# Performance work log

Measured on AMD Instinct MI355X. Metric: run time of the kernel, lower is better.

Reference implementation:

```python
import jax, jax.numpy as jnp
import numpy as np

N_HEAD = 16
N_KV_HEADS = 4
HEAD_DIM = 64  # n_emb // n_head = 1024 // 16
WINDOW = 512
NEG_INF = float('-inf')


def _rope_tables(T, dim, dtype):
    inv_freq = 1.0 / (10000.0 ** (jnp.arange(0, dim, 2, dtype=jnp.float32) / dim))
    t = jnp.arange(T, dtype=jnp.float32)
    freqs = jnp.einsum('i,j->ij', t, inv_freq)          # [T, dim/2]
    emb = jnp.concatenate((freqs, freqs), axis=-1)       # [T, dim]
    return jnp.cos(emb).astype(dtype), jnp.sin(emb).astype(dtype)


def _apply_rope(x, cos, sin):
    # x: [B, H, T, D]; cos/sin: [T, D]
    x1, x2 = jnp.split(x, 2, axis=-1)
    x_rot = jnp.concatenate((-x2, x1), axis=-1)
    return x * cos + x_rot * sin


def setup_inputs() -> dict:
    key = jax.random.key(0)
    ks = jax.random.split(key, 5)
    B, T, C = 1, 4096, 1024
    kv_dim = N_KV_HEADS * HEAD_DIM
    s = 0.02
    return {
        'x': jax.random.normal(ks[0], (B, T, C), jnp.float32),
        'wq': jax.random.normal(ks[1], (C, C), jnp.float32) * s,
        'wk': jax.random.normal(ks[2], (kv_dim, C), jnp.float32) * s,
        'wv': jax.random.normal(ks[3], (kv_dim, C), jnp.float32) * s,
        'wo': jax.random.normal(ks[4], (C, C), jnp.float32) * s,
    }


def reference(x, wq, wk, wv, wo):
    B, T, C = x.shape
    n_rep = N_HEAD // N_KV_HEADS
    # QKV projections (torch Linear: x @ W.T)
    q = (x @ wq.T).reshape(B, T, N_HEAD, HEAD_DIM).transpose(0, 2, 1, 3)      # [B,H,T,D]
    k = (x @ wk.T).reshape(B, T, N_KV_HEADS, HEAD_DIM).transpose(0, 2, 1, 3)  # [B,Hkv,T,D]
    v = (x @ wv.T).reshape(B, T, N_KV_HEADS, HEAD_DIM).transpose(0, 2, 1, 3)
    # RoPE
    cos, sin = _rope_tables(T, HEAD_DIM, x.dtype)
    q = _apply_rope(q, cos, sin)
    k = _apply_rope(k, cos, sin)
    # GQA: repeat KV heads
    k = jnp.repeat(k, n_rep, axis=1)  # [B,H,T,D]
    v = jnp.repeat(v, n_rep, axis=1)
    # Sliding-window causal mask: allow j <= i and j > i - WINDOW
    i = jnp.arange(T)[:, None]
    j = jnp.arange(T)[None, :]
    allowed = (j <= i) & (j > i - WINDOW)  # [T,T]
    scale = 1.0 / np.sqrt(HEAD_DIM)
    scores = jnp.einsum('bhqd,bhkd->bhqk', q, k) * scale
    scores = jnp.where(allowed[None, None], scores, NEG_INF)
    attn = jax.nn.softmax(scores, axis=-1)
    y = jnp.einsum('bhqk,bhkd->bhqd', attn, v)            # [B,H,T,D]
    y = y.transpose(0, 2, 1, 3).reshape(B, T, C)
    return y @ wo.T
```

## Files before the change

### kernel.cpp

```cpp
#include <hip/hip_runtime.h>
#include <hip/hip_bf16.h>
#include <stdint.h>

#define T_SEQ 4096
#define CDIM  1024
#define NH    16
#define NKV   4
#define HD    64
#define WIN   512
#define KVD   256
#define QKVN  1536

typedef unsigned short ushort_t;
typedef __attribute__((ext_vector_type(8))) __bf16 bf16x8;
typedef __attribute__((ext_vector_type(4))) float  f32x4;
typedef __attribute__((ext_vector_type(4))) unsigned short us4;
typedef __attribute__((ext_vector_type(8))) unsigned short us8;

__device__ inline unsigned short f2bf(float f) {
  unsigned u = __builtin_bit_cast(unsigned, f);
  u += 0x7fffu + ((u >> 16) & 1u);
  return (unsigned short)(u >> 16);
}

__device__ inline unsigned cvt_pk_bf16(float lo, float hi) {
  unsigned r;
  asm("v_cvt_pk_bf16_f32 %0, %1, %2" : "=v"(r) : "v"(lo), "v"(hi));
  return r;
}

__device__ inline f32x4 mfma16(bf16x8 a, bf16x8 b, f32x4 c) {
  return __builtin_amdgcn_mfma_f32_16x16x32_bf16(a, b, c, 0, 0, 0);
}

__device__ inline void load_lds16(const void* g, void* s) {
  __builtin_amdgcn_global_load_lds(
      (const __attribute__((address_space(1))) void*)g,
      (__attribute__((address_space(3))) void*)s, 16, 0, 0);
}

__global__ __launch_bounds__(256) void prep_kernel(
    const float* __restrict__ x,  const float* __restrict__ wq,
    const float* __restrict__ wk, const float* __restrict__ wv,
    const float* __restrict__ wo,
    ushort_t* __restrict__ xb, ushort_t* __restrict__ wqkvb,
    ushort_t* __restrict__ wob,
    float* __restrict__ ct, float* __restrict__ st) {
  const int NX  = T_SEQ * CDIM / 8;
  const int NWQ = CDIM * CDIM / 8;
  const int NWK = KVD * CDIM / 8;
  const int NCONV = NX + 2 * NWQ + 2 * NWK;
  int i = blockIdx.x * 256 + threadIdx.x;
  if (i >= NCONV) {
    int j = i - NCONV;
    if (j >= T_SEQ * 32) return;
    int t = j >> 5, f = j & 31;
    float inv = __builtin_exp2f(-(float)f * (13.287712379549449f / 32.0f));
    float a = (float)t * inv;
    ct[j] = cosf(a);
    st[j] = sinf(a);
    return;
  }
  const float4* src; ushort_t* dst; int off;
  if (i < NX)                        { src = (const float4*)x;  dst = xb;                              off = i; }
  else if (i < NX + NWQ)             { src = (const float4*)wq; dst = wqkvb;                           off = i - NX; }
  else if (i < NX + NWQ + NWK)       { src = (const float4*)wk; dst = wqkvb + CDIM * CDIM;             off = i - NX - NWQ; }
  else if (i < NX + NWQ + 2 * NWK)   { src = (const float4*)wv; dst = wqkvb + CDIM * CDIM + KVD * CDIM; off = i - NX - NWQ - NWK; }
  else                               { src = (const float4*)wo; dst = wob;                             off = i - NX - NWQ - 2 * NWK; }
  float4 v0 = src[off * 2], v1 = src[off * 2 + 1];
  us8 o;
  o[0] = f2bf(v0.x); o[1] = f2bf(v0.y); o[2] = f2bf(v0.z); o[3] = f2bf(v0.w);
  o[4] = f2bf(v1.x); o[5] = f2bf(v1.y); o[6] = f2bf(v1.z); o[7] = f2bf(v1.w);
  *(us8*)(dst + (size_t)off * 8) = o;
}

template <int EPI>
__global__ __launch_bounds__(256) void gemm_kernel(
    const ushort_t* __restrict__ A, const ushort_t* __restrict__ B, int K,
    float* __restrict__ outF,
    ushort_t* __restrict__ qbuf, ushort_t* __restrict__ kbuf, ushort_t* __restrict__ vt,
    const float* __restrict__ ct, const float* __restrict__ st) {
  __shared__ __align__(16) ushort_t smA[2][64 * 64];
  __shared__ __align__(16) ushort_t smB[2][128 * 64];
  const int tid = threadIdx.x, lane = tid & 63, wid = tid >> 6;

  const int id = blockIdx.x + (gridDim.x * blockIdx.y);
  const int nwg = gridDim.x * gridDim.y;
  const int swz = (id & 7) * (nwg >> 3) + (id >> 3);
  const int bm = (swz & 63) * 64, bn = (swz >> 6) * 128;

  const int wr = wid >> 1, wc = wid & 1;
  const int l15 = lane & 15, lg = lane >> 4;
  const int r8 = lane >> 3;
  const int cc = lane & 7;
  const int scc = (cc ^ r8) * 8;

  f32x4 acc[2][4];
#pragma unroll
  for (int i = 0; i < 2; i++)
#pragma unroll
    for (int j = 0; j < 4; j++) acc[i][j] = (f32x4)0.0f;

#define GSTAGE(buf, ktv)                                                                              \
  do {                                                                                                \
    load_lds16(A + (size_t)(bm + wid * 8 + r8) * K + (ktv) + scc, (char*)smA[buf] + wid * 1024);                 \
    load_lds16(A + (size_t)(bm + (wid + 4) * 8 + r8) * K + (ktv) + scc, (char*)smA[buf] + (wid + 4) * 1024);     \
    load_lds16(B + (size_t)(bn + wid * 8 + r8) * K + (ktv) + scc, (char*)smB[buf] + wid * 1024);                 \
    load_lds16(B + (size_t)(bn + (wid + 4) * 8 + r8) * K + (ktv) + scc, (char*)smB[buf] + (wid + 4) * 1024);     \
    load_lds16(B + (size_t)(bn + (wid + 8) * 8 + r8) * K + (ktv) + scc, (char*)smB[buf] + (wid + 8) * 1024);     \
    load_lds16(B + (size_t)(bn + (wid + 12) * 8 + r8) * K + (ktv) + scc, (char*)smB[buf] + (wid + 12) * 1024);   \
  } while (0)

  GSTAGE(0, 0);
  const int NK = K / 64;
  int cur = 0;
  for (int kt = 0; kt < NK; ++kt) {
    if (kt + 1 < NK) {
      GSTAGE(cur ^ 1, (kt + 1) * 64);
      asm volatile("s_waitcnt vmcnt(6)" ::: "memory");
    } else {
      asm volatile("s_waitcnt vmcnt(0)" ::: "memory");
    }
    __builtin_amdgcn_sched_barrier(0);
    __builtin_amdgcn_s_barrier();
    __builtin_amdgcn_sched_barrier(0);

    bf16x8 af[2][2], bfr[4][2];
#pragma unroll
    for (int mi = 0; mi < 2; mi++) {
      int r = wr * 32 + mi * 16 + l15, sw8 = r & 7;
#pragma unroll
      for (int ks = 0; ks < 2; ks++)
        af[mi][ks] = *(const bf16x8*)&smA[cur][r * 64 + ((ks * 4 + lg) ^ sw8) * 8];
    }
#pragma unroll
    for (int ni = 0; ni < 4; ni++) {
      int r = wc * 64 + ni * 16 + l15, sw8 = r & 7;
#pragma unroll
      for (int ks = 0; ks < 2; ks++)
        bfr[ni][ks] = *(const bf16x8*)&smB[cur][r * 64 + ((ks * 4 + lg) ^ sw8) * 8];
    }
#pragma unroll
    for (int ks = 0; ks < 2; ks++)
#pragma unroll
      for (int mi = 0; mi < 2; mi++)
#pragma unroll
        for (int ni = 0; ni < 4; ni++)
          acc[mi][ni] = mfma16(af[mi][ks], bfr[ni][ks], acc[mi][ni]);

    __builtin_amdgcn_sched_barrier(0);
    __builtin_amdgcn_s_barrier();
    __builtin_amdgcn_sched_barrier(0);
    cur ^= 1;
  }
#undef GSTAGE

  const int col0 = bn + wc * 64;
  if (EPI == 1) {
#pragma unroll
    for (int mi = 0; mi < 2; mi++) {
      int r0 = bm + wr * 32 + mi * 16 + lg * 4;
#pragma unroll
      for (int ni = 0; ni < 4; ni++) {
        int c = col0 + ni * 16 + l15;
#pragma unroll
        for (int r = 0; r < 4; r++) outF[(size_t)(r0 + r) * CDIM + c] = acc[mi][ni][r];
      }
    }
  } else {
    if (col0 < CDIM + KVD) {
      bool isQ = (col0 < CDIM);
      ushort_t* obuf = isQ ? qbuf : kbuf;
      int ostride = isQ ? CDIM : KVD;
      int obase = isQ ? col0 : col0 - CDIM;
#pragma unroll
      for (int mi = 0; mi < 2; mi++) {
        int r0 = bm + wr * 32 + mi * 16 + lg * 4;
#pragma unroll
        for (int ni = 0; ni < 2; ni++) {
          int dd = ni * 16 + l15;
#pragma unroll
          for (int r = 0; r < 4; r++) {
            int t = r0 + r;
            float c_ = ct[t * 32 + dd], s_ = st[t * 32 + dd];
            float lo = acc[mi][ni][r], hi = acc[mi][ni + 2][r];
            obuf[(size_t)t * ostride + obase + dd]      = f2bf(lo * c_ - hi * s_);
            obuf[(size_t)t * ostride + obase + dd + 32] = f2bf(hi * c_ + lo * s_);
          }
        }
      }
    } else {
#pragma unroll
      for (int mi = 0; mi < 2; mi++) {
        int t0 = bm + wr * 32 + mi * 16 + lg * 4;
#pragma unroll
        for (int ni = 0; ni < 4; ni++) {
          int cv = col0 + ni * 16 + l15 - (CDIM + KVD);
          us4 o;
          o.x = f2bf(acc[mi][ni][0]); o.y = f2bf(acc[mi][ni][1]);
          o.z = f2bf(acc[mi][ni][2]); o.w = f2bf(acc[mi][ni][3]);
          *(us4*)&vt[(size_t)cv * T_SEQ + t0] = o;
        }
      }
    }
  }
}

__global__ __launch_bounds__(256, 4) void attn_kernel(
    const ushort_t* __restrict__ qbuf, const ushort_t* __restrict__ kbuf,
    const ushort_t* __restrict__ vt, ushort_t* __restrict__ ybuf) {
  __shared__ __align__(16) ushort_t smK[2][64 * 64];
  __shared__ __align__(16) ushort_t smV[2][64 * 64];
  const int tid = threadIdx.x, lane = tid & 63, wid = tid >> 6;
  const int l15 = lane & 15, lg = lane >> 4;
  const int blk = blockIdx.x;
  const int h  = (blk & 7) * 2 + ((blk >> 3) & 1);
  const int qb = (blk >> 4) * 64;
  const int kvh = h >> 2;
  const int qbw = qb + wid * 16;

  const int r8 = lane >> 3;
  const int cc = lane & 7;
  const int sc = ((cc ^ r8) * 8);
  const int ra = wid * 8 + r8;
  const int rb = (wid + 4) * 8 + r8;

  int kb0 = qb - (WIN - 1);
  if (kb0 < 0) kb0 = 0;
  kb0 &= ~63;
  const int nt = ((qb + 63) - kb0) / 64 + 1;

#define STAGE(buf, kbase)                                                                  \
  do {                                                                                     \
    load_lds16(kbuf + (size_t)((kbase) + ra) * KVD + kvh * HD + sc, (char*)smK[buf] + wid * 1024);        \
    load_lds16(kbuf + (size_t)((kbase) + rb) * KVD + kvh * HD + sc, (char*)smK[buf] + (wid + 4) * 1024);  \
    load_lds16(vt + (size_t)(kvh * HD + ra) * T_SEQ + (kbase) + sc, (char*)smV[buf] + wid * 1024);        \
    load_lds16(vt + (size_t)(kvh * HD + rb) * T_SEQ + (kbase) + sc, (char*)smV[buf] + (wid + 4) * 1024);  \
  } while (0)

  STAGE(0, kb0);

  const ushort_t* qrow = qbuf + (size_t)(qbw + l15) * CDIM + h * HD;
  bf16x8 qf0 = *(const bf16x8*)(qrow + lg * 8);
  bf16x8 qf1 = *(const bf16x8*)(qrow + 32 + lg * 8);

  f32x4 o[4];
#pragma unroll
  for (int j = 0; j < 4; j++) o[j] = (f32x4)0.f;
  float lpart = 0.f;
  const float SC = 0.125f * 1.4426950408889634f;
  const int sw = l15 & 7;

  int cur = 0;
  for (int t = 0; t < nt; ++t) {
    const int kb = kb0 + t * 64;
    if (t + 1 < nt) {
      STAGE(cur ^ 1, kb + 64);
      asm volatile("s_waitcnt vmcnt(4)" ::: "memory");
    } else {
      asm volatile("s_waitcnt vmcnt(0)" ::: "memory");
    }
    __builtin_amdgcn_sched_barrier(0);
    __builtin_amdgcn_s_barrier();
    __builtin_amdgcn_sched_barrier(0);

    if (kb <= qbw + 15) {
      const ushort_t* sk = smK[cur];
      const ushort_t* sv_ = smV[cur];

      f32x4 s[4];
      __builtin_amdgcn_s_setprio(1);
#pragma unroll
      for (int g = 0; g < 4; g++) {
        bf16x8 k0 = *(const bf16x8*)&sk[(g * 16 + l15) * 64 + ((lg ^ sw) * 8)];
        bf16x8 k1 = *(const bf16x8*)&sk[(g * 16 + l15) * 64 + (((4 + lg) ^ sw) * 8)];
        s[g] = mfma16(k0, qf0, (f32x4)0.f);
        s[g] = mfma16(k1, qf1, s[g]);
      }
      __builtin_amdgcn_s_setprio(0);

      const bool nomask = (kb + 63 <= qbw) && (kb > qbw + 15 - WIN);
      unsigned pw[8];
      {
        const int q = qbw + l15;
        float ps = 0.f;
#pragma unroll
        for (int g = 0; g < 4; g++) {
          float p0, p1, p2, p3;
          if (nomask) {
            p0 = __builtin_exp2f(s[g][0] * SC);
            p1 = __builtin_exp2f(s[g][1] * SC);
            p2 = __builtin_exp2f(s[g][2] * SC);
            p3 = __builtin_exp2f(s[g][3] * SC);
          } else {
            int k0 = kb + g * 16 + lg * 4;
            p0 = __builtin_exp2f((k0 + 0 <= q && k0 + 0 > q - WIN) ? s[g][0] * SC : -3e38f);
            p1 = __builtin_exp2f((k0 + 1 <= q && k0 + 1 > q - WIN) ? s[g][1] * SC : -3e38f);
            p2 = __builtin_exp2f((k0 + 2 <= q && k0 + 2 > q - WIN) ? s[g][2] * SC : -3e38f);
            p3 = __builtin_exp2f((k0 + 3 <= q && k0 + 3 > q - WIN) ? s[g][3] * SC : -3e38f);
          }
          ps += (p0 + p1) + (p2 + p3);
          pw[g * 2 + 0] = cvt_pk_bf16(p0, p1);
          pw[g * 2 + 1] = cvt_pk_bf16(p2, p3);
        }
        lpart += ps;
      }

      asm("v_permlane32_swap_b32 %0, %1" : "+v"(pw[0]), "+v"(pw[2]));
      asm("v_permlane32_swap_b32 %0, %1" : "+v"(pw[1]), "+v"(pw[3]));
      asm("v_permlane32_swap_b32 %0, %1" : "+v"(pw[4]), "+v"(pw[6]));
      asm("v_permlane32_swap_b32 %0, %1" : "+v"(pw[5]), "+v"(pw[7]));
      asm("v_permlane16_swap_b32 %0, %1" : "+v"(pw[0]), "+v"(pw[2]));
      asm("v_permlane16_swap_b32 %0, %1" : "+v"(pw[1]), "+v"(pw[3]));
      asm("v_permlane16_swap_b32 %0, %1" : "+v"(pw[4]), "+v"(pw[6]));
      asm("v_permlane16_swap_b32 %0, %1" : "+v"(pw[5]), "+v"(pw[7]));
      bf16x8 pf0, pf1;
      {
        union { unsigned u[4]; bf16x8 v; } c0, c1;
        c0.u[0] = pw[0]; c0.u[1] = pw[1]; c0.u[2] = pw[2]; c0.u[3] = pw[3];
        c1.u[0] = pw[4]; c1.u[1] = pw[5]; c1.u[2] = pw[6]; c1.u[3] = pw[7];
        pf0 = c0.v;
        pf1 = c1.v;
      }

      __builtin_amdgcn_s_setprio(1);
#pragma unroll
      for (int n = 0; n < 4; n++) {
        bf16x8 v0 = *(const bf16x8*)&sv_[(n * 16 + l15) * 64 + ((lg ^ sw) * 8)];
        bf16x8 v1 = *(const bf16x8*)&sv_[(n * 16 + l15) * 64 + (((4 + lg) ^ sw) * 8)];
        o[n] = mfma16(pf0, v0, o[n]);
        o[n] = mfma16(pf1, v1, o[n]);
      }
      __builtin_amdgcn_s_setprio(0);
    }
    __builtin_amdgcn_sched_barrier(0);
    __builtin_amdgcn_s_barrier();
    __builtin_amdgcn_sched_barrier(0);
    cur ^= 1;
  }
#undef STAGE

  {
    float l = lpart;
    l += __shfl_xor(l, 16);
    l += __shfl_xor(l, 32);
    float inv = 1.f / l;
    float i0 = __shfl(inv, lg * 4 + 0);
    float i1 = __shfl(inv, lg * 4 + 1);
    float i2 = __shfl(inv, lg * 4 + 2);
    float i3 = __shfl(inv, lg * 4 + 3);
    ushort_t* yb = ybuf + (size_t)qbw * CDIM + h * HD;
#pragma unroll
    for (int r = 0; r < 4; r++) {
      float ir = (r == 0) ? i0 : (r == 1) ? i1 : (r == 2) ? i2 : i3;
      size_t t = lg * 4 + r;
      yb[t * CDIM + 0  + l15] = f2bf(o[0][r] * ir);
      yb[t * CDIM + 16 + l15] = f2bf(o[1][r] * ir);
      yb[t * CDIM + 32 + l15] = f2bf(o[2][r] * ir);
      yb[t * CDIM + 48 + l15] = f2bf(o[3][r] * ir);
    }
  }
}

extern "C" void kernel_launch(void* const* d_in, const int* in_sizes, int n_in,
                              void* d_out, int out_size, void* d_ws, size_t ws_size,
                              hipStream_t stream) {
  const float* x  = (const float*)d_in[0];
  const float* wq = (const float*)d_in[1];
  const float* wk = (const float*)d_in[2];
  const float* wv = (const float*)d_in[3];
  const float* wo = (const float*)d_in[4];
  float* out = (float*)d_out;

  char* ws = (char*)d_ws;
  ushort_t* xb    = (ushort_t*)(ws + 0);
  ushort_t* wqkvb = (ushort_t*)(ws + 8388608);
  ushort_t* wob   = (ushort_t*)(ws + 11534336);
  ushort_t* qbuf  = (ushort_t*)(ws + 13631488);
  ushort_t* kbuf  = (ushort_t*)(ws + 22020096);
  ushort_t* vt    = (ushort_t*)(ws + 24117248);
  ushort_t* ybuf  = (ushort_t*)(ws + 26214400);
  float*    ct    = (float*)(ws + 34603008);
  float*    st    = (float*)(ws + 35127296);

  prep_kernel<<<3840, 256, 0, stream>>>(x, wq, wk, wv, wo, xb, wqkvb, wob, ct, st);

  dim3 g1(64, 12);
  gemm_kernel<0><<<g1, 256, 0, stream>>>(xb, wqkvb, CDIM, nullptr, qbuf, kbuf, vt, ct, st);

  attn_kernel<<<1024, 256, 0, stream>>>(qbuf, kbuf, vt, ybuf);

  dim3 g2(64, 8);
  gemm_kernel<1><<<g2, 256, 0, stream>>>(ybuf, wob, CDIM, out, nullptr, nullptr, nullptr, nullptr, nullptr);
}
```

Baseline: 72.66 us.

## Add dedicated output-projection GEMM with K=128 tiles and split A/B buffering

Replaces the templated output-projection GEMM with a specialized kernel that uses 128-wide K tiles. A is double-buffered and B single-buffered, and the next B tile is loaded right after the fragments are read into registers. This halves the number of K iterations and barriers, which cuts loop overhead and synchronisation in the final GEMM. In exchange it uses more LDS per block, caps occupancy at two blocks per SM via launch bounds, and holds more fragment registers.

```diff
diff --git a/kernel.cpp b/kernel.cpp
--- a/kernel.cpp
+++ b/kernel.cpp
@@ -74,10 +74,8 @@
   *(us8*)(dst + (size_t)off * 8) = o;
 }
 
-template <int EPI>
 __global__ __launch_bounds__(256) void gemm_kernel(
     const ushort_t* __restrict__ A, const ushort_t* __restrict__ B, int K,
-    float* __restrict__ outF,
     ushort_t* __restrict__ qbuf, ushort_t* __restrict__ kbuf, ushort_t* __restrict__ vt,
     const float* __restrict__ ct, const float* __restrict__ st) {
   __shared__ __align__(16) ushort_t smA[2][64 * 64];
@@ -156,52 +154,142 @@
 #undef GSTAGE
 
   const int col0 = bn + wc * 64;
-  if (EPI == 1) {
+  if (col0 < CDIM + KVD) {
+    bool isQ = (col0 < CDIM);
+    ushort_t* obuf = isQ ? qbuf : kbuf;
+    int ostride = isQ ? CDIM : KVD;
+    int obase = isQ ? col0 : col0 - CDIM;
 #pragma unroll
     for (int mi = 0; mi < 2; mi++) {
       int r0 = bm + wr * 32 + mi * 16 + lg * 4;
 #pragma unroll
+      for (int ni = 0; ni < 2; ni++) {
+        int dd = ni * 16 + l15;
+#pragma unroll
+        for (int r = 0; r < 4; r++) {
+          int t = r0 + r;
+          float c_ = ct[t * 32 + dd], s_ = st[t * 32 + dd];
+          float lo = acc[mi][ni][r], hi = acc[mi][ni + 2][r];
+          obuf[(size_t)t * ostride + obase + dd]      = f2bf(lo * c_ - hi * s_);
+          obuf[(size_t)t * ostride + obase + dd + 32] = f2bf(hi * c_ + lo * s_);
+        }
+      }
+    }
+  } else {
+#pragma unroll
+    for (int mi = 0; mi < 2; mi++) {
+      int t0 = bm + wr * 32 + mi * 16 + lg * 4;
+#pragma unroll
       for (int ni = 0; ni < 4; ni++) {
-        int c = col0 + ni * 16 + l15;
-#pragma unroll
-        for (int r = 0; r < 4; r++) outF[(size_t)(r0 + r) * CDIM + c] = acc[mi][ni][r];
-      }
-    }
-  } else {
-    if (col0 < CDIM + KVD) {
-      bool isQ = (col0 < CDIM);
-      ushort_t* obuf = isQ ? qbuf : kbuf;
-      int ostride = isQ ? CDIM : KVD;
-      int obase = isQ ? col0 : col0 - CDIM;
-#pragma unroll
-      for (int mi = 0; mi < 2; mi++) {
-        int r0 = bm + wr * 32 + mi * 16 + lg * 4;
-#pragma unroll
-        for (int ni = 0; ni < 2; ni++) {
-          int dd = ni * 16 + l15;
-#pragma unroll
-          for (int r = 0; r < 4; r++) {
-            int t = r0 + r;
-            float c_ = ct[t * 32 + dd], s_ = st[t * 32 + dd];
-            float lo = acc[mi][ni][r], hi = acc[mi][ni + 2][r];
-            obuf[(size_t)t * ostride + obase + dd]      = f2bf(lo * c_ - hi * s_);
-            obuf[(size_t)t * ostride + obase + dd + 32] = f2bf(hi * c_ + lo * s_);
-          }
-        }
-      }
+        int cv = col0 + ni * 16 + l15 - (CDIM + KVD);
+        us4 o;
+        o.x = f2bf(acc[mi][ni][0]); o.y = f2bf(acc[mi][ni][1]);
+        o.z = f2bf(acc[mi][ni][2]); o.w = f2bf(acc[mi][ni][3]);
+        *(us4*)&vt[(size_t)cv * T_SEQ + t0] = o;
+      }
+    }
+  }
+}
+
+__global__ __launch_bounds__(256, 2) void gemm1_kernel(
+    const ushort_t* __restrict__ A, const ushort_t* __restrict__ B,
+    float* __restrict__ outF) {
+  const int K = CDIM;
+  __shared__ __align__(16) ushort_t smA[2][64 * 128];
+  __shared__ __align__(16) ushort_t smB[128 * 128];
+  const int tid = threadIdx.x, lane = tid & 63, wid = tid >> 6;
+
+  const int id = blockIdx.x + (gridDim.x * blockIdx.y);
+  const int nwg = gridDim.x * gridDim.y;
+  const int swz = (id & 7) * (nwg >> 3) + (id >> 3);
+  const int bm = (swz & 63) * 64, bn = (swz >> 6) * 128;
+
+  const int wr = wid >> 1, wc = wid & 1;
+  const int l15 = lane & 15, lg = lane >> 4;
+  const int r4 = lane >> 4;
+  const int c16 = lane & 15;
+
+  f32x4 acc[2][4];
+#pragma unroll
+  for (int i = 0; i < 2; i++)
+#pragma unroll
+    for (int j = 0; j < 4; j++) acc[i][j] = (f32x4)0.0f;
+
+#define G1A(buf, ktv)                                                                         \
+  do {                                                                                        \
+    _Pragma("unroll") for (int j = 0; j < 4; ++j) {                                           \
+      int inst = wid * 4 + j; int R = inst * 4 + r4;                                          \
+      load_lds16(A + (size_t)(bm + R) * K + (ktv) + ((c16 ^ (R & 15)) * 8),                   \
+                 (char*)smA[buf] + inst * 1024);                                              \
+    }                                                                                         \
+  } while (0)
+#define G1B(ktv)                                                                              \
+  do {                                                                                        \
+    _Pragma("unroll") for (int j = 0; j < 8; ++j) {                                           \
+      int inst = wid * 8 + j; int R = inst * 4 + r4;                                          \
+      load_lds16(B + (size_t)(bn + R) * K + (ktv) + ((c16 ^ (R & 15)) * 8),                   \
+                 (char*)smB + inst * 1024);                                                   \
+    }                                                                                         \
+  } while (0)
+
+  G1A(0, 0);
+  G1B(0);
+  const int NK = K / 128;
+  int cur = 0;
+  for (int kt = 0; kt < NK; ++kt) {
+    if (kt + 1 < NK) {
+      G1A(cur ^ 1, (kt + 1) * 128);
+      asm volatile("s_waitcnt vmcnt(4)" ::: "memory");
     } else {
-#pragma unroll
-      for (int mi = 0; mi < 2; mi++) {
-        int t0 = bm + wr * 32 + mi * 16 + lg * 4;
-#pragma unroll
-        for (int ni = 0; ni < 4; ni++) {
-          int cv = col0 + ni * 16 + l15 - (CDIM + KVD);
-          us4 o;
-          o.x = f2bf(acc[mi][ni][0]); o.y = f2bf(acc[mi][ni][1]);
-          o.z = f2bf(acc[mi][ni][2]); o.w = f2bf(acc[mi][ni][3]);
-          *(us4*)&vt[(size_t)cv * T_SEQ + t0] = o;
-        }
-      }
+      asm volatile("s_waitcnt vmcnt(0)" ::: "memory");
+    }
+    __builtin_amdgcn_sched_barrier(0);
+    __builtin_amdgcn_s_barrier();
+    __builtin_amdgcn_sched_barrier(0);
+
+    bf16x8 af[2][4], bfr[4][4];
+#pragma unroll
+    for (int mi = 0; mi < 2; mi++) {
+      int r = wr * 32 + mi * 16 + l15, rs = r & 15;
+#pragma unroll
+      for (int ks = 0; ks < 4; ks++)
+        af[mi][ks] = *(const bf16x8*)&smA[cur][r * 128 + ((ks * 4 + lg) ^ rs) * 8];
+    }
+#pragma unroll
+    for (int ni = 0; ni < 4; ni++) {
+      int r = wc * 64 + ni * 16 + l15, rs = r & 15;
+#pragma unroll
+      for (int ks = 0; ks < 4; ks++)
+        bfr[ni][ks] = *(const bf16x8*)&smB[r * 128 + ((ks * 4 + lg) ^ rs) * 8];
+    }
+    asm volatile("s_waitcnt lgkmcnt(0)" ::: "memory");
+    __builtin_amdgcn_sched_barrier(0);
+    __builtin_amdgcn_s_barrier();
+    __builtin_amdgcn_sched_barrier(0);
+    if (kt + 1 < NK) G1B((kt + 1) * 128);
+    __builtin_amdgcn_sched_barrier(0);
+
+#pragma unroll
+    for (int ks = 0; ks < 4; ks++)
+#pragma unroll
+      for (int mi = 0; mi < 2; mi++)
+#pragma unroll
+        for (int ni = 0; ni < 4; ni++)
+          acc[mi][ni] = mfma16(af[mi][ks], bfr[ni][ks], acc[mi][ni]);
+    cur ^= 1;
+  }
+#undef G1A
+#undef G1B
+
+  const int col0 = bn + wc * 64;
+#pragma unroll
+  for (int mi = 0; mi < 2; mi++) {
+    int r0 = bm + wr * 32 + mi * 16 + lg * 4;
+#pragma unroll
+    for (int ni = 0; ni < 4; ni++) {
+      int c = col0 + ni * 16 + l15;
+#pragma unroll
+      for (int r = 0; r < 4; r++) outF[(size_t)(r0 + r) * CDIM + c] = acc[mi][ni][r];
     }
   }
 }
@@ -386,10 +474,10 @@
   prep_kernel<<<3840, 256, 0, stream>>>(x, wq, wk, wv, wo, xb, wqkvb, wob, ct, st);
 
   dim3 g1(64, 12);
-  gemm_kernel<0><<<g1, 256, 0, stream>>>(xb, wqkvb, CDIM, nullptr, qbuf, kbuf, vt, ct, st);
+  gemm_kernel<<<g1, 256, 0, stream>>>(xb, wqkvb, CDIM, qbuf, kbuf, vt, ct, st);
 
   attn_kernel<<<1024, 256, 0, stream>>>(qbuf, kbuf, vt, ybuf);
 
   dim3 g2(64, 8);
-  gemm_kernel<1><<<g2, 256, 0, stream>>>(ybuf, wob, CDIM, out, nullptr, nullptr, nullptr, nullptr, nullptr);
-}
+  gemm1_kernel<<<g2, 256, 0, stream>>>(ybuf, wob, out);
+}
```

Result: no change. 73.37 us (+1.0%).
